# Kernel optimization log

Hardware: AMD Instinct MI355X
Metric: run time of the kernel (lower is better)

The kernel has to match this reference:

```python
import jax, jax.numpy as jnp
import numpy as np

B, S, D, H = 4, 2048, 1024, 16
HD = D // H


def setup_inputs() -> dict:
    key = jax.random.key(0)
    k1, k2, k3 = jax.random.split(key, 3)
    x = jax.random.normal(k1, (B, S, D), dtype=jnp.float32)
    w_qkv = jax.random.normal(k2, (D, 3 * D), dtype=jnp.float32) * (1.0 / np.sqrt(D))
    w_out = jax.random.normal(k3, (D, D), dtype=jnp.float32) * (1.0 / np.sqrt(D))
    return {"x": x, "w_qkv": w_qkv, "w_out": w_out}


def reference(x, w_qkv, w_out):
    bsz, seq_len, d = x.shape
    qkv = x @ w_qkv  # [B, S, 3D]
    q, k, v = jnp.split(qkv, 3, axis=-1)
    # [B, H, S, HD]
    q = q.reshape(bsz, seq_len, H, HD).transpose(0, 2, 1, 3)
    k = k.reshape(bsz, seq_len, H, HD).transpose(0, 2, 1, 3)
    v = v.reshape(bsz, seq_len, H, HD).transpose(0, 2, 1, 3)
    scale = 1.0 / np.sqrt(HD)
    scores = jnp.einsum('bhqd,bhkd->bhqk', q, k) * scale  # [B, H, S, S]
    causal = jnp.tril(jnp.ones((seq_len, seq_len), dtype=bool))
    scores = jnp.where(causal[None, None], scores, -jnp.inf)
    weights = jax.nn.softmax(scores, axis=-1)
    ctx = jnp.einsum('bhqk,bhkd->bhqd', weights, v)
    ctx = ctx.transpose(0, 2, 1, 3).reshape(bsz, seq_len, d)
    return ctx @ w_out
```

## Files before the change

kernel.cpp:

```cpp
#include <hip/hip_runtime.h>
#include <stdint.h>

typedef unsigned short u16;
typedef __attribute__((ext_vector_type(4))) float f32x4;
typedef __attribute__((ext_vector_type(8))) __bf16 bf16x8;
typedef __attribute__((ext_vector_type(8))) u16 u16x8;
typedef __attribute__((ext_vector_type(4))) u16 u16x4;
typedef __attribute__((ext_vector_type(2))) unsigned u32x2;

static constexpr int kB = 4, kS = 2048, kD = 1024, kH = 16, kHD = 64;
static constexpr int M1 = kB * kS;
static constexpr int N1 = 3 * kD;
static constexpr int K1 = kD;

#define SCLF 0.18033688011112042f
#define MFMA16(a, b, c) __builtin_amdgcn_mfma_f32_16x16x32_bf16((a), (b), (c), 0, 0, 0)

union U4 { unsigned u[4]; bf16x8 v; };

__device__ __forceinline__ u16 f2bf(float f) {
  union { float f; uint32_t u; } c; c.f = f;
  uint32_t u = c.u + 0x7FFFu + ((c.u >> 16) & 1u);
  return (u16)(u >> 16);
}

__device__ __forceinline__ unsigned pkbf(float a, float b) {
  union { __bf16 h[2]; unsigned u; } c;
  c.h[0] = (__bf16)a; c.h[1] = (__bf16)b;
  return c.u;
}

__device__ __forceinline__ float max3f(float a, float b, float c) {
  return fmaxf(fmaxf(a, b), c);
}

__device__ __forceinline__ void gload_lds16(const u16* g, u16* l) {
  __builtin_amdgcn_global_load_lds(
      (const __attribute__((address_space(1))) unsigned int*)g,
      (__attribute__((address_space(3))) unsigned int*)l, 16, 0, 0);
}

__global__ __launch_bounds__(256) void k_prep(const float* __restrict__ x,
                                              const float* __restrict__ w_qkv,
                                              const float* __restrict__ w_out,
                                              u16* __restrict__ x_bf,
                                              u16* __restrict__ wqkvT,
                                              u16* __restrict__ woutT) {
  const int bid = blockIdx.x;
  if (bid < 8192) {
    int i = (bid * 256 + threadIdx.x) * 4;
    f32x4 v = *(const f32x4*)(x + i);
    u16x4 r;
    r[0] = f2bf(v[0]); r[1] = f2bf(v[1]); r[2] = f2bf(v[2]); r[3] = f2bf(v[3]);
    *(u16x4*)(x_bf + i) = r;
    return;
  }
  __shared__ float t[32][33];
  const float* w; u16* wt; int N, idx;
  if (bid < 8192 + 3072) { idx = bid - 8192;  w = w_qkv; wt = wqkvT; N = N1; }
  else                   { idx = bid - 11264; w = w_out; wt = woutT; N = kD; }
  const int ntn = N >> 5;
  const int n0 = (idx % ntn) * 32, k0 = (idx / ntn) * 32;
  const int tx = threadIdx.x & 31, ty = threadIdx.x >> 5;
  for (int r = ty; r < 32; r += 8)
    t[r][tx] = w[(size_t)(k0 + r) * N + n0 + tx];
  __syncthreads();
  for (int r = ty; r < 32; r += 8)
    wt[(size_t)(n0 + r) * K1 + k0 + tx] = f2bf(t[tx][r]);
}

template <int MODE>
__global__ __launch_bounds__(512) void k_gemm_bt(const u16* __restrict__ A,
                                                 const u16* __restrict__ BT,
                                                 u16* __restrict__ obf,
                                                 float* __restrict__ of,
                                                 int M, int N, int K) {
  __shared__ __align__(16) u16 Asb[3][128 * 64];
  __shared__ __align__(16) u16 Bsb[3][256 * 64];

  const int tid = threadIdx.x;
  const int wave = tid >> 6, lane = tid & 63;
  const int l15 = lane & 15, l16 = lane >> 4;

  const int bid = blockIdx.x;
  const int qch = gridDim.x >> 3;
  const int swz = (bid & 7) * qch + (bid >> 3);
  const int ntN = N >> 8;
  const int row0 = (swz / ntN) * 128, col0 = (swz % ntN) * 256;
  const int wm = (wave >> 2) * 64, wn = (wave & 3) * 64;

  f32x4 acc[4][4];
#pragma unroll
  for (int i = 0; i < 4; ++i)
#pragma unroll
    for (int j = 0; j < 4; ++j) acc[i][j] = f32x4{0.f, 0.f, 0.f, 0.f};

  const int lr = lane >> 3, ls = lane & 7;
  const u16* srcA[2];
#pragma unroll
  for (int j = 0; j < 2; ++j) {
    const int r = (wave * 2 + j) * 8 + lr;
    srcA[j] = A + (size_t)(row0 + r) * K + (ls ^ (r & 7)) * 8;
  }
  const u16* srcB[4];
#pragma unroll
  for (int j = 0; j < 4; ++j) {
    const int r = (wave * 4 + j) * 8 + lr;
    srcB[j] = BT + (size_t)(col0 + r) * K + (ls ^ (r & 7)) * 8;
  }

  const int nT = K >> 6;

#define STAGE(t)                                                        \
  {                                                                     \
    const int buf_ = (t) % 3;                                           \
    const int kt_ = (t) * 64;                                           \
    _Pragma("unroll")                                                   \
    for (int j = 0; j < 2; ++j)                                         \
      gload_lds16(srcA[j] + kt_, &Asb[buf_][(wave * 2 + j) * 512]);     \
    _Pragma("unroll")                                                   \
    for (int j = 0; j < 4; ++j)                                         \
      gload_lds16(srcB[j] + kt_, &Bsb[buf_][(wave * 4 + j) * 512]);     \
  }

  STAGE(0);
  STAGE(1);

  for (int t = 0; t < nT; ++t) {
    if (t + 1 < nT) asm volatile("s_waitcnt vmcnt(6)" ::: "memory");
    else            asm volatile("s_waitcnt vmcnt(0)" ::: "memory");
    __builtin_amdgcn_s_barrier();
    __builtin_amdgcn_sched_barrier(0);

    if (t + 2 < nT) STAGE(t + 2);

    const u16* As = &Asb[t % 3][0];
    const u16* Bs = &Bsb[t % 3][0];
#pragma unroll
    for (int kk = 0; kk < 2; ++kk) {
      bf16x8 af[4], bfv[4];
#pragma unroll
      for (int f = 0; f < 4; ++f) {
        const int ra = wm + f * 16 + l15;
        af[f] = *(const bf16x8*)&As[ra * 64 + (((kk * 4 + l16) ^ (ra & 7)) * 8)];
        const int rb = wn + f * 16 + l15;
        bfv[f] = *(const bf16x8*)&Bs[rb * 64 + (((kk * 4 + l16) ^ (rb & 7)) * 8)];
      }
      __builtin_amdgcn_s_setprio(1);
#pragma unroll
      for (int fm = 0; fm < 4; ++fm)
#pragma unroll
        for (int fn = 0; fn < 4; ++fn)
          acc[fm][fn] = MFMA16(af[fm], bfv[fn], acc[fm][fn]);
      __builtin_amdgcn_s_setprio(0);
    }
  }

#pragma unroll
  for (int fm = 0; fm < 4; ++fm)
#pragma unroll
    for (int fn = 0; fn < 4; ++fn) {
      const int n = col0 + wn + fn * 16 + l15;
#pragma unroll
      for (int j = 0; j < 4; ++j) {
        const int m = row0 + wm + fm * 16 + l16 * 4 + j;
        float v = acc[fm][fn][j];
        if constexpr (MODE == 0) {
          const int which = n >> 10, d = n & 1023;
          const int h = d >> 6, hd = d & 63;
          const int b = m >> 11, s = m & 2047;
          if (which == 0) v *= SCLF;
          obf[((((size_t)which * 4 + b) * 16 + h) * 2048 + s) * 64 + hd] = f2bf(v);
        } else {
          of[(size_t)m * N + n] = v;
        }
      }
    }
#undef STAGE
}

__global__ __launch_bounds__(512, 4) void k_attn(const u16* __restrict__ Qg,
                                                 const u16* __restrict__ Kg,
                                                 const u16* __restrict__ Vg,
                                                 u16* __restrict__ ctx) {
  __shared__ __align__(16) u16 Ks[2][64 * 64];
  __shared__ __align__(16) unsigned Vt[2][2048];
  __shared__ __align__(16) unsigned Pl[8 * 256];

  const int bid = blockIdx.x;
  const int xcd = bid & 7, i2 = bid >> 3;
  const int bh = xcd * 8 + (i2 & 7);
  const int p = i2 >> 3;
  const int bb = bh >> 4, hh = bh & 15;
  const int tid = threadIdx.x;
  const int wave = tid >> 6, lane = tid & 63;
  const int l15 = lane & 15, l16 = lane >> 4;

  const u16* Qb = Qg + (size_t)bh * kS * kHD;
  const u16* Kb = Kg + (size_t)bh * kS * kHD;
  const u16* Vb = Vg + (size_t)bh * kS * kHD;

  const int kkey = tid >> 3, ksl = tid & 7;
  const int do4 = tid & 15, kp = tid >> 4;
  unsigned* Pw = Pl + wave * 256 + l15 * 16;
  const int pm = ((l15 >> 1) & 3) << 2;

  U4 onesu;
#pragma unroll
  for (int i = 0; i < 4; ++i) onesu.u[i] = 0x3F803F80u;
  const bf16x8 vones = onesu.v;

  unsigned voff[4];
#pragma unroll
  for (int i = 0; i < 4; ++i) {
    const int d = do4 * 4 + i;
    voff[i] = d * 32 + (kp ^ ((((d & 7) ^ (d >> 3))) << 2));
  }
  const u16* ksrc = Kb + (size_t)kkey * 64 + (ksl ^ (kkey & 7)) * 8;

  for (int phase = 0; phase < 2; ++phase) {
    const int qsup = phase ? (15 - p) : p;
    const int qstart = qsup * 128 + wave * 16;
    const int ntiles = 2 * qsup + 2;

    bf16x8 bq[2];
#pragma unroll
    for (int ds = 0; ds < 2; ++ds)
      bq[ds] = *(const bf16x8*)(Qb + (size_t)(qstart + l15) * 64 + ds * 32 + l16 * 8);

    f32x4 acc[4];
#pragma unroll
    for (int i = 0; i < 4; ++i) acc[i] = f32x4{0.f, 0.f, 0.f, 0.f};
    f32x4 acc_l = f32x4{0.f, 0.f, 0.f, 0.f};
    float mrow = -3e38f;

    __syncthreads();

    u16x4 va, vb;
    {
      const u16* vs = Vb + (size_t)(2 * kp) * 64 + do4 * 4;
      va = *(const u16x4*)vs; vb = *(const u16x4*)(vs + 64);
    }
#pragma unroll
    for (int i = 0; i < 4; ++i)
      Vt[0][voff[i]] = (unsigned)va[i] | ((unsigned)vb[i] << 16);
    {
      const u16* vs = Vb + (size_t)(64 + 2 * kp) * 64 + do4 * 4;
      va = *(const u16x4*)vs; vb = *(const u16x4*)(vs + 64);
    }
    gload_lds16(ksrc, &Ks[0][wave * 512]);

    for (int t = 0; t < ntiles; ++t) {
      const int kv0 = t * 64;
      __syncthreads();

      if (t + 1 < ntiles) {
        const int nb = (t + 1) & 1;
#pragma unroll
        for (int i = 0; i < 4; ++i)
          Vt[nb][voff[i]] = (unsigned)va[i] | ((unsigned)vb[i] << 16);
        gload_lds16(ksrc + (size_t)(t + 1) * 64 * 64, &Ks[nb][wave * 512]);
        if (t + 2 < ntiles) {
          const u16* vs = Vb + (size_t)((t + 2) * 64 + 2 * kp) * 64 + do4 * 4;
          va = *(const u16x4*)vs; vb = *(const u16x4*)(vs + 64);
        }
      }

      if (kv0 > qstart + 15) continue;

      const u16* Ksb = &Ks[t & 1][0];
      const unsigned* Vtb = &Vt[t & 1][0];
      const int qv = qstart + l15;
      const bool have1 = (kv0 + 32 <= qstart + 15);

      f32x4 stA0 = f32x4{0.f, 0.f, 0.f, 0.f}, stA1 = stA0;
      f32x4 stB0 = stA0, stB1 = stA0;
      __builtin_amdgcn_s_setprio(1);
#pragma unroll
      for (int ds = 0; ds < 2; ++ds) {
        const int slot = ((ds * 4 + l16) ^ (l15 & 7)) * 8;
        bf16x8 ak0 = *(const bf16x8*)&Ksb[(l15) * 64 + slot];
        stA0 = MFMA16(ak0, bq[ds], stA0);
        bf16x8 ak1 = *(const bf16x8*)&Ksb[(16 + l15) * 64 + slot];
        stA1 = MFMA16(ak1, bq[ds], stA1);
        if (have1) {
          bf16x8 bk0 = *(const bf16x8*)&Ksb[(32 + l15) * 64 + slot];
          stB0 = MFMA16(bk0, bq[ds], stB0);
          bf16x8 bk1 = *(const bf16x8*)&Ksb[(48 + l15) * 64 + slot];
          stB1 = MFMA16(bk1, bq[ds], stB1);
        }
      }
      __builtin_amdgcn_s_setprio(0);

      if (kv0 + 31 > qstart) {
#pragma unroll
        for (int j = 0; j < 4; ++j) {
          const int key = kv0 + l16 * 4 + j;
          stA0[j] = (key <= qv) ? stA0[j] : -3e38f;
          stA1[j] = (key + 16 <= qv) ? stA1[j] : -3e38f;
        }
      }
      if (have1 && (kv0 + 63 > qstart)) {
#pragma unroll
        for (int j = 0; j < 4; ++j) {
          const int key = kv0 + 32 + l16 * 4 + j;
          stB0[j] = (key <= qv) ? stB0[j] : -3e38f;
          stB1[j] = (key + 16 <= qv) ? stB1[j] : -3e38f;
        }
      }

      float tl;
      {
        const float mA = fmaxf(max3f(stA0[0], stA0[1], stA0[2]),
                               max3f(stA0[3], stA1[0], stA1[1]));
        tl = max3f(stA1[2], stA1[3], mA);
        if (have1) {
          const float mB = fmaxf(max3f(stB0[0], stB0[1], stB0[2]),
                                 max3f(stB0[3], stB1[0], stB1[1]));
          tl = fmaxf(tl, max3f(stB1[2], stB1[3], mB));
        }
      }

      float mn;
      if (__all(tl <= mrow + 8.0f)) {
        mn = mrow;
      } else {
        float tj = fmaxf(tl, __shfl_xor(tl, 16, 64));
        tj = fmaxf(tj, __shfl_xor(tj, 32, 64));
        mn = fmaxf(mrow, tj);
        const float al = exp2f(mrow - mn);
        mrow = mn;
        acc_l[0] *= al;
#pragma unroll
        for (int i = 0; i < 4; ++i)
#pragma unroll
          for (int j = 0; j < 4; ++j) acc[i][j] *= al;
      }

      {
#pragma unroll
        for (int j = 0; j < 4; ++j) {
          stA0[j] = exp2f(stA0[j] - mn);
          stA1[j] = exp2f(stA1[j] - mn);
        }
        const unsigned p0 = pkbf(stA0[0], stA0[1]);
        const unsigned p1 = pkbf(stA0[2], stA0[3]);
        const unsigned p2 = pkbf(stA1[0], stA1[1]);
        const unsigned p3 = pkbf(stA1[2], stA1[3]);
        *(u32x2*)&Pw[(l16 * 2) ^ pm] = u32x2{p0, p1};
        *(u32x2*)&Pw[(8 + l16 * 2) ^ pm] = u32x2{p2, p3};
        U4 f;
        f = *(const U4*)&Pw[(l16 * 4) ^ pm];
        __builtin_amdgcn_s_setprio(1);
        acc_l = MFMA16(vones, f.v, acc_l);
#pragma unroll
        for (int dg = 0; dg < 4; ++dg) {
          const int d = dg * 16 + l15;
          const int addr = d * 32 + ((l16 * 4) ^ ((((d & 7) ^ (d >> 3))) << 2));
          const bf16x8 vf = *(const bf16x8*)&Vtb[addr];
          acc[dg] = MFMA16(vf, f.v, acc[dg]);
        }
        __builtin_amdgcn_s_setprio(0);
      }
      if (have1) {
#pragma unroll
        for (int j = 0; j < 4; ++j) {
          stB0[j] = exp2f(stB0[j] - mn);
          stB1[j] = exp2f(stB1[j] - mn);
        }
        const unsigned p0 = pkbf(stB0[0], stB0[1]);
        const unsigned p1 = pkbf(stB0[2], stB0[3]);
        const unsigned p2 = pkbf(stB1[0], stB1[1]);
        const unsigned p3 = pkbf(stB1[2], stB1[3]);
        *(u32x2*)&Pw[(l16 * 2) ^ pm] = u32x2{p0, p1};
        *(u32x2*)&Pw[(8 + l16 * 2) ^ pm] = u32x2{p2, p3};
        U4 f;
        f = *(const U4*)&Pw[(l16 * 4) ^ pm];
        __builtin_amdgcn_s_setprio(1);
        acc_l = MFMA16(vones, f.v, acc_l);
#pragma unroll
        for (int dg = 0; dg < 4; ++dg) {
          const int d = dg * 16 + l15;
          const int addr = d * 32 + ((16 + l16 * 4) ^ ((((d & 7) ^ (d >> 3))) << 2));
          const bf16x8 vf = *(const bf16x8*)&Vtb[addr];
          acc[dg] = MFMA16(vf, f.v, acc[dg]);
        }
        __builtin_amdgcn_s_setprio(0);
      }
    }

    const float rl = 1.0f / acc_l[0];
    u16* orow = ctx + ((size_t)bb * kS + (qstart + l15)) * kD + hh * 64;
#pragma unroll
    for (int dg = 0; dg < 4; ++dg) {
      u16x4 pk;
#pragma unroll
      for (int j = 0; j < 4; ++j) pk[j] = f2bf(acc[dg][j] * rl);
      *(u16x4*)&orow[dg * 16 + l16 * 4] = pk;
    }
  }
}

extern "C" void kernel_launch(void* const* d_in, const int* in_sizes, int n_in,
                              void* d_out, int out_size, void* d_ws, size_t ws_size,
                              hipStream_t stream) {
  const float* x     = (const float*)d_in[0];
  const float* w_qkv = (const float*)d_in[1];
  const float* w_out = (const float*)d_in[2];
  float* out = (float*)d_out;

  u16* ws    = (u16*)d_ws;
  u16* x_bf  = ws;
  u16* wqkvT = x_bf + (size_t)M1 * K1;
  u16* woutT = wqkvT + (size_t)N1 * K1;
  u16* qkv   = woutT + (size_t)kD * kD;
  u16* ctx   = qkv + (size_t)3 * kB * kH * kS * kHD;

  k_prep<<<dim3(12288), 256, 0, stream>>>(x, w_qkv, w_out, x_bf, wqkvT, woutT);

  k_gemm_bt<0><<<dim3(768), 512, 0, stream>>>(x_bf, wqkvT, qkv, nullptr,
                                              M1, N1, K1);

  const u16* Qg = qkv;
  const u16* Kg = qkv + (size_t)kB * kH * kS * kHD;
  const u16* Vg = qkv + (size_t)2 * kB * kH * kS * kHD;
  k_attn<<<dim3(512), 512, 0, stream>>>(Qg, Kg, Vg, ctx);

  k_gemm_bt<1><<<dim3(256), 512, 0, stream>>>(ctx, woutT, nullptr, out,
                                              M1, kD, K1);
}
```

Measured before the change: 197.6 us.

## Interleave global prefetch with LDS reads and MFMA phases in GEMM mainloop

Restructures the GEMM main loop into two half-K phases. Each phase issues its LDS fragment reads, then a share of the next-stage global-to-LDS loads, and is separated from the next phase by explicit barriers and sched_barriers, in a ping-pong style schedule. The aim is to spread memory issue across the MFMA work and lower scheduling stalls. The cost is more barriers per iteration, and the wait-count logic becomes more fragile.

Result: faster. 181.6 us (-8.1%).

```diff
diff --git a/kernel.cpp b/kernel.cpp
--- a/kernel.cpp
+++ b/kernel.cpp
@@ -125,35 +125,70 @@
 
   STAGE(0);
   STAGE(1);
+  asm volatile("s_waitcnt vmcnt(6)" ::: "memory");
+  __builtin_amdgcn_s_barrier();
 
   for (int t = 0; t < nT; ++t) {
-    if (t + 1 < nT) asm volatile("s_waitcnt vmcnt(6)" ::: "memory");
-    else            asm volatile("s_waitcnt vmcnt(0)" ::: "memory");
-    __builtin_amdgcn_s_barrier();
-    __builtin_amdgcn_sched_barrier(0);
-
-    if (t + 2 < nT) STAGE(t + 2);
-
     const u16* As = &Asb[t % 3][0];
     const u16* Bs = &Bsb[t % 3][0];
-#pragma unroll
-    for (int kk = 0; kk < 2; ++kk) {
-      bf16x8 af[4], bfv[4];
-#pragma unroll
-      for (int f = 0; f < 4; ++f) {
-        const int ra = wm + f * 16 + l15;
-        af[f] = *(const bf16x8*)&As[ra * 64 + (((kk * 4 + l16) ^ (ra & 7)) * 8)];
-        const int rb = wn + f * 16 + l15;
-        bfv[f] = *(const bf16x8*)&Bs[rb * 64 + (((kk * 4 + l16) ^ (rb & 7)) * 8)];
-      }
-      __builtin_amdgcn_s_setprio(1);
-#pragma unroll
-      for (int fm = 0; fm < 4; ++fm)
-#pragma unroll
-        for (int fn = 0; fn < 4; ++fn)
-          acc[fm][fn] = MFMA16(af[fm], bfv[fn], acc[fm][fn]);
-      __builtin_amdgcn_s_setprio(0);
-    }
+    const bool pf = (t + 2 < nT);
+    const int buf2 = (t + 2) % 3;
+    const int kt2 = (t + 2) * 64;
+    bf16x8 af[4], bfv[4];
+
+#pragma unroll
+    for (int f = 0; f < 4; ++f) {
+      const int ra = wm + f * 16 + l15;
+      af[f] = *(const bf16x8*)&As[ra * 64 + ((l16 ^ (ra & 7)) * 8)];
+      const int rb = wn + f * 16 + l15;
+      bfv[f] = *(const bf16x8*)&Bs[rb * 64 + ((l16 ^ (rb & 7)) * 8)];
+    }
+    if (pf) {
+      gload_lds16(srcA[0] + kt2, &Asb[buf2][(wave * 2 + 0) * 512]);
+      gload_lds16(srcA[1] + kt2, &Asb[buf2][(wave * 2 + 1) * 512]);
+      gload_lds16(srcB[0] + kt2, &Bsb[buf2][(wave * 4 + 0) * 512]);
+    }
+    __builtin_amdgcn_sched_barrier(0);
+    __builtin_amdgcn_s_barrier();
+    asm volatile("s_waitcnt lgkmcnt(0)" ::: "memory");
+    __builtin_amdgcn_sched_barrier(0);
+    __builtin_amdgcn_s_setprio(1);
+#pragma unroll
+    for (int fm = 0; fm < 4; ++fm)
+#pragma unroll
+      for (int fn = 0; fn < 4; ++fn)
+        acc[fm][fn] = MFMA16(af[fm], bfv[fn], acc[fm][fn]);
+    __builtin_amdgcn_s_setprio(0);
+    __builtin_amdgcn_sched_barrier(0);
+    __builtin_amdgcn_s_barrier();
+
+#pragma unroll
+    for (int f = 0; f < 4; ++f) {
+      const int ra = wm + f * 16 + l15;
+      af[f] = *(const bf16x8*)&As[ra * 64 + (((4 + l16) ^ (ra & 7)) * 8)];
+      const int rb = wn + f * 16 + l15;
+      bfv[f] = *(const bf16x8*)&Bs[rb * 64 + (((4 + l16) ^ (rb & 7)) * 8)];
+    }
+    if (pf) {
+      gload_lds16(srcB[1] + kt2, &Bsb[buf2][(wave * 4 + 1) * 512]);
+      gload_lds16(srcB[2] + kt2, &Bsb[buf2][(wave * 4 + 2) * 512]);
+      gload_lds16(srcB[3] + kt2, &Bsb[buf2][(wave * 4 + 3) * 512]);
+    }
+    if (pf)                asm volatile("s_waitcnt vmcnt(6)" ::: "memory");
+    else if (t + 1 < nT)   asm volatile("s_waitcnt vmcnt(0)" ::: "memory");
+    __builtin_amdgcn_sched_barrier(0);
+    __builtin_amdgcn_s_barrier();
+    asm volatile("s_waitcnt lgkmcnt(0)" ::: "memory");
+    __builtin_amdgcn_sched_barrier(0);
+    __builtin_amdgcn_s_setprio(1);
+#pragma unroll
+    for (int fm = 0; fm < 4; ++fm)
+#pragma unroll
+      for (int fn = 0; fn < 4; ++fn)
+        acc[fm][fn] = MFMA16(af[fm], bfv[fn], acc[fm][fn]);
+    __builtin_amdgcn_s_setprio(0);
+    __builtin_amdgcn_sched_barrier(0);
+    __builtin_amdgcn_s_barrier();
   }
 
 #pragma unroll
```
